# Kernel tuning notes

Hardware: AMD Instinct MI355X
Metric: run time of the kernel (lower is better)

The kernel has to match this reference:

```python
import jax, jax.numpy as jnp
from jax import lax
import numpy as np

EPSILON = 0.5
BETA = 1.0
N_ITER_FREE = 500
N_ITER_CLAMPED = 8


def setup_inputs() -> dict:
    key = jax.random.key(0)
    ks = jax.random.split(key, 12)
    B = 256
    x = jax.random.uniform(ks[0], (B, 784), dtype=jnp.float32)
    t = jax.random.uniform(ks[1], (B, 10), dtype=jnp.float32)
    u1 = jnp.zeros((B, 500), jnp.float32)
    u2 = jnp.zeros((B, 500), jnp.float32)
    u3 = jnp.zeros((B, 500), jnp.float32)
    u4 = jnp.zeros((B, 10), jnp.float32)
    a0 = np.float32(np.sqrt(2.0 / (784.0 + 500.0)))
    a1 = np.float32(np.sqrt(2.0 / (500.0 + 500.0)))
    a2 = np.float32(np.sqrt(2.0 / (500.0 + 10.0)))
    W0 = jax.random.normal(ks[2], (784, 500), jnp.float32) * a0
    b0 = jax.random.normal(ks[3], (500,), jnp.float32) * a0
    W1 = jax.random.normal(ks[4], (500, 500), jnp.float32) * a1
    b1 = jax.random.normal(ks[5], (500,), jnp.float32) * a1
    W2 = jax.random.normal(ks[6], (500, 500), jnp.float32) * a1
    b2 = jax.random.normal(ks[7], (500,), jnp.float32) * a1
    W3 = jax.random.normal(ks[8], (500, 10), jnp.float32) * a2
    b3 = jax.random.normal(ks[9], (10,), jnp.float32) * a2
    return dict(x=x, u1=u1, u2=u2, u3=u3, u4=u4, t=t,
                W0=W0, W1=W1, W2=W2, W3=W3, b0=b0, b1=b1, b2=b2, b3=b3)


def _rho(v):
    return jnp.clip(v, 0.0, 1.0)


def _d_rho(v):
    return ((v >= 0.0) & (v <= 1.0)).astype(v.dtype)


def reference(x, u1, u2, u3, u4, t, W0, W1, W2, W3, b0, b1, b2, b3):
    # x (units[0]) is clamped input; precompute its constant drive into layer 1.
    xW0 = x @ W0 + b0  # [B,500], invariant across iterations

    def deltas(c):
        u1, u2, u3, u4 = c
        # Jacobi update: all d_units use the pre-update states (matches torch code).
        d1 = _d_rho(u1) * (xW0 + u2 @ W1.T) - u1
        d2 = _d_rho(u2) * (u1 @ W1 + u3 @ W2.T + b1) - u2
        d3 = _d_rho(u3) * (u2 @ W2 + u4 @ W3.T + b2) - u3
        d4 = _d_rho(u4) * (u3 @ W3 + b3) - u4
        return d1, d2, d3, d4

    def free_step(c, _):
        d1, d2, d3, d4 = deltas(c)
        new = tuple(_rho(u + EPSILON * d) for u, d in zip(c, (d1, d2, d3, d4)))
        return new, None

    def clamped_step(c, _):
        d1, d2, d3, d4 = deltas(c)
        d4 = d4 + BETA * (t - c[3])
        new = tuple(_rho(u + EPSILON * d) for u, d in zip(c, (d1, d2, d3, d4)))
        return new, None

    units_free, _ = lax.scan(free_step, (u1, u2, u3, u4), None, length=N_ITER_FREE)
    units_clamped, _ = lax.scan(clamped_step, units_free, None, length=N_ITER_CLAMPED)
    # fixed_points returns (units_free, units_clamped); flatten the two phases.
    return (*units_free, *units_clamped)
```

## Files before the change

### kernel.cpp

```cpp
#include <hip/hip_runtime.h>


typedef float  f32x4 __attribute__((ext_vector_type(4)));
typedef short  s16x8 __attribute__((ext_vector_type(8)));
typedef short  s16x4 __attribute__((ext_vector_type(4)));
typedef unsigned int uint;
typedef uint   u32x4 __attribute__((ext_vector_type(4)));

#define MFMA_BF16 __builtin_amdgcn_mfma_f32_16x16x32_bf16

#define NFREE   500
#define NCLAMP  8
#define NITER   (NFREE + NCLAMP)
#define ROWLEN  1568
#define NSAMP   256
#define ROWTOT  (NSAMP * ROWLEN)

#define B1_OFF   0
#define B2A_OFF  262144
#define B2B_OFF  524288
#define B3A_OFF  786432
#define B3B_OFF  1048576
#define B4_OFF   1064960
#define BTOT     1081344

#define WS_UHL   0
#define WS_XW0   (WS_UHL + 2*ROWTOT*4)
#define WS_BIAS  (WS_XW0 + NSAMP*512*4)
#define WS_CNT   (WS_BIAS + 6400)
#define WS_BH    (WS_CNT + 1024)
#define WS_BL    (WS_BH + BTOT*2)
#define WS_END   (WS_BL + BTOT*2)

__device__ __forceinline__ short f2bf(float f){
  unsigned u = __float_as_uint(f);
  unsigned r = (u + 0x7FFFu + ((u >> 16) & 1u)) >> 16;
  return (short)r;
}
__device__ __forceinline__ float bf2f(short s){
  return __uint_as_float(((unsigned)(unsigned short)s) << 16);
}
__device__ __forceinline__ uint packbf(float v){
  short h = f2bf(v);
  short l = f2bf(v - bf2f(h));
  return (uint)(unsigned short)h | ((uint)(unsigned short)l << 16);
}

#define SYSLD(dst, addr) \
  asm volatile("global_load_dwordx4 %0, %1, off sc0 sc1" : "=v"(dst) : "v"(addr) : "memory")
__device__ __forceinline__ void store_sys(uint* p, uint v){
  asm volatile("global_store_dword %0, %1, off sc0 sc1" :: "v"(p), "v"(v) : "memory");
}
#define VMW_(N, X) do { \
  asm volatile("s_waitcnt vmcnt(" #N ")\n//%0" : "+v"(X) :: "memory"); \
  __builtin_amdgcn_sched_barrier(0); } while(0)
#define VMW(N, X) VMW_(N, X)
#define PRC(N, X, OFF) do { \
  VMW(N, X); \
  s16x4 h_ = (s16x4){ (short)((X)[0] & 0xffff), (short)((X)[1] & 0xffff), \
                      (short)((X)[2] & 0xffff), (short)((X)[3] & 0xffff) }; \
  s16x4 l_ = (s16x4){ (short)((X)[0] >> 16), (short)((X)[1] >> 16), \
                      (short)((X)[2] >> 16), (short)((X)[3] >> 16) }; \
  *(s16x4*)(L + (OFF)) = h_; *(s16x4*)(L + 32768 + (OFF)) = l_; } while(0)

#define BARRIER(ITV) do { \
  asm volatile("s_waitcnt vmcnt(0)" ::: "memory"); \
  __syncthreads(); \
  if (tid == 0){ \
    __hip_atomic_fetch_add(cg, 1u, __ATOMIC_RELAXED, __HIP_MEMORY_SCOPE_SYSTEM); \
    const unsigned tgt_ = 16u * (unsigned)((ITV) + 1); \
    while (__hip_atomic_load(cg, __ATOMIC_RELAXED, __HIP_MEMORY_SCOPE_SYSTEM) < tgt_){ \
      __builtin_amdgcn_s_sleep(1); \
    } \
  } \
  __syncthreads(); } while(0)

__global__ void initK(const float* __restrict__ u1, const float* __restrict__ u2,
                      const float* __restrict__ u3, const float* __restrict__ u4,
                      const float* __restrict__ b1, const float* __restrict__ b2,
                      uint* __restrict__ uhl, float* __restrict__ bias,
                      uint* __restrict__ cnt){
  const int b = blockIdx.x, tid = threadIdx.x;
  for (int col = tid; col < ROWLEN; col += 256){
    float v;
    if      (col < 512)  v = (col < 500)        ? u1[b*500 + col]        : 0.f;
    else if (col < 1024) v = ((col-512) < 500)  ? u2[b*500 + col - 512]  : 0.f;
    else if (col < 1536) v = ((col-1024) < 500) ? u3[b*500 + col - 1024] : 0.f;
    else                 v = ((col-1536) < 10)  ? u4[b*10 + col - 1536]  : 0.f;
    uhl[b*ROWLEN + col] = packbf(v);
    if (b == 0){
      float bv = 0.f;
      if      (col >= 512  && col < 1024){ int i = col-512;  if (i < 500) bv = b1[i]; }
      else if (col >= 1024 && col < 1536){ int i = col-1024; if (i < 500) bv = b2[i]; }
      bias[col] = bv;
    }
  }
  if (b == 0) cnt[tid] = 0;
}

__global__ void xw0K(const float* __restrict__ x, const float* __restrict__ W0,
                     const float* __restrict__ b0, float* __restrict__ xw0p){
  __shared__ float xs[784];
  const int b = blockIdx.x, tid = threadIdx.x;
  for (int j = tid; j < 784; j += 512) xs[j] = x[b*784 + j];
  __syncthreads();
  float a = 0.f;
  if (tid < 500){
    a = b0[tid];
    #pragma unroll 4
    for (int j = 0; j < 784; ++j) a = fmaf(xs[j], W0[j*500 + tid], a);
  }
  xw0p[b*512 + tid] = (tid < 500) ? a : 0.f;
}

__global__ void packK(const float* __restrict__ W1, const float* __restrict__ W2,
                      const float* __restrict__ W3, short* __restrict__ Bh,
                      short* __restrict__ Bl){
  const int bid = blockIdx.x, ln = threadIdx.x;
  int m, base, nks, poff;
  if      (bid < 512) { m=0; base=0;    nks=16; poff=B1_OFF;  }
  else if (bid < 1024){ m=1; base=512;  nks=16; poff=B2A_OFF; }
  else if (bid < 1536){ m=2; base=1024; nks=16; poff=B2B_OFF; }
  else if (bid < 2048){ m=3; base=1536; nks=16; poff=B3A_OFF; }
  else if (bid < 2080){ m=4; base=2048; nks=1;  poff=B3B_OFF; }
  else                { m=5; base=2080; nks=16; poff=B4_OFF;  }
  const int local = bid - base, ct = local / nks, ks = local % nks;
  short hv[8], lv[8];
  #pragma unroll
  for (int j = 0; j < 8; ++j){
    const int k = ks*32 + (ln>>4)*8 + j;
    const int c = ct*16 + (ln & 15);
    float v = 0.f;
    if      (m==0){ if (k<500 && c<500) v = W1[c*500 + k]; }
    else if (m==1){ if (k<500 && c<500) v = W1[k*500 + c]; }
    else if (m==2){ if (k<500 && c<500) v = W2[c*500 + k]; }
    else if (m==3){ if (k<500 && c<500) v = W2[k*500 + c]; }
    else if (m==4){ if (k<10  && c<500) v = W3[c*10  + k]; }
    else          { if (k<500 && c<10 ) v = W3[k*10  + c]; }
    short h = f2bf(v); hv[j] = h; lv[j] = f2bf(v - bf2f(h));
  }
  const int o = poff + (ct*nks + ks)*512 + ln*8;
  #pragma unroll
  for (int j = 0; j < 8; ++j){ Bh[o+j] = hv[j]; Bl[o+j] = lv[j]; }
}

__global__ void __launch_bounds__(256, 1) mainK(
    const short* __restrict__ Bh, const short* __restrict__ Bl,
    uint* __restrict__ uhl, const float* __restrict__ xw0p,
    const float* __restrict__ bias,
    const float* __restrict__ u1in, const float* __restrict__ u2in,
    const float* __restrict__ u3in, const float* __restrict__ u4in,
    const float* __restrict__ tin, const float* __restrict__ b3,
    float* __restrict__ dout, uint* __restrict__ cnt)
{
  __shared__ short ldss[32768];
  char* L = (char*)ldss;
  const int bid = blockIdx.x;
  const int rg  = bid & 15;
  const int tp  = bid >> 4;
  const int tid = threadIdx.x;
  const int wv  = tid >> 6, ln = tid & 63;
  const int lrow = ln & 15, lkg = ln >> 4;
  const int rowbase = rg * 16;
  const int sg16 = tid >> 4, l16 = tid & 15;
  const int abase = lrow*2048 + ((lkg*16) ^ ((lrow & 7) << 4));
  uint* cg = cnt + rg*16;

  if (tp < 8){
    s16x8 bh[32], bl[32];
    const int ctg = tp*4 + wv;
    #pragma unroll
    for (int ks = 0; ks < 32; ++ks){
      const int of = (ks < 16 ? B2A_OFF + (ctg*16 + ks)*512
                              : B2B_OFF + (ctg*16 + ks - 16)*512) + ln*8;
      bh[ks] = *(const s16x8*)(Bh + of);
      bl[ks] = *(const s16x8*)(Bl + of);
    }
    const int i0 = tp*64 + wv*16 + lrow;
    const int colg = 512 + i0;
    const float biasv = bias[colg];
    f32x4 uold, uold4;
    #pragma unroll
    for (int r = 0; r < 4; ++r){
      const int b = rowbase + lkg*4 + r;
      uold[r]  = (i0 < 500)   ? u2in[b*500 + i0]  : 0.f;
      uold4[r] = (lrow < 10)  ? u4in[b*10 + lrow] : 0.f;
    }
    const int rA = sg16 >> 1, half = sg16 & 1;
    const bool doU4 = (tp == 0 && wv == 0);

    for (int it = 0; it < NITER; ++it){
      const uint* uhlB = uhl + (size_t)(it & 1)*ROWTOT;
      uint*       uhlN = uhl + (size_t)((it & 1) ^ 1)*ROWTOT;
      const int snap = (it == NFREE-1) ? 0 : ((it == NITER-1) ? 386560 : -1);
      {
        const uint* sA = uhlB + (size_t)(rowbase + rA)*ROWLEN + half*1024 + l16*4;
        const uint* sB = sA + 8*ROWLEN;
        u32x4 a0,a1,a2,a3,a4,a5,a6,a7,c0,c1,c2,c3,c4,c5,c6,c7;
        SYSLD(a0, sA+0);   SYSLD(a1, sA+64);  SYSLD(a2, sA+128); SYSLD(a3, sA+192);
        SYSLD(a4, sA+256); SYSLD(a5, sA+320); SYSLD(a6, sA+384); SYSLD(a7, sA+448);
        SYSLD(c0, sB+0);   SYSLD(c1, sB+64);  SYSLD(c2, sB+128); SYSLD(c3, sB+192);
        SYSLD(c4, sB+256); SYSLD(c5, sB+320); SYSLD(c6, sB+384); SYSLD(c7, sB+448);
        const int obA = rA*2048 + ((half*1024 + l16*8) ^ ((rA & 7) << 4));
        const int obB = obA + 16384;
        PRC(15, a0, obA+0);   PRC(14, a1, obA+128); PRC(13, a2, obA+256); PRC(12, a3, obA+384);
        PRC(11, a4, obA+512); PRC(10, a5, obA+640); PRC(9,  a6, obA+768); PRC(8,  a7, obA+896);
        PRC(7,  c0, obB+0);   PRC(6,  c1, obB+128); PRC(5,  c2, obB+256); PRC(4,  c3, obB+384);
        PRC(3,  c4, obB+512); PRC(2,  c5, obB+640); PRC(1,  c6, obB+768); PRC(0,  c7, obB+896);
      }
      __syncthreads();
      f32x4 acc = {0.f,0.f,0.f,0.f};
      #pragma unroll
      for (int ks = 0; ks < 32; ++ks){
        const int off = abase ^ (ks*64);
        s16x8 aH = *(const s16x8*)(L + off);
        s16x8 aL = *(const s16x8*)(L + 32768 + off);
        acc = MFMA_BF16(aH, bh[ks], acc, 0, 0, 0);
        acc = MFMA_BF16(aH, bl[ks], acc, 0, 0, 0);
        acc = MFMA_BF16(aL, bh[ks], acc, 0, 0, 0);
      }
      f32x4 acc4 = {0.f,0.f,0.f,0.f};
      if (doU4){
        #pragma unroll
        for (int ks = 0; ks < 16; ++ks){
          const int off = (abase + 1024) ^ (ks*64);
          s16x8 aH = *(const s16x8*)(L + off);
          s16x8 aL = *(const s16x8*)(L + 32768 + off);
          const int of4 = B4_OFF + ks*512 + ln*8;
          s16x8 b4h = *(const s16x8*)(Bh + of4);
          s16x8 b4l = *(const s16x8*)(Bl + of4);
          acc4 = MFMA_BF16(aH, b4h, acc4, 0, 0, 0);
          acc4 = MFMA_BF16(aH, b4l, acc4, 0, 0, 0);
          acc4 = MFMA_BF16(aL, b4h, acc4, 0, 0, 0);
        }
      }
      #pragma unroll
      for (int r = 0; r < 4; ++r){
        const int b = rowbase + lkg*4 + r;
        const float y = acc[r] + biasv;
        float v = 0.5f*(uold[r] + y);
        v = fminf(fmaxf(v, 0.f), 1.f);
        if (i0 >= 500) v = 0.f;
        uold[r] = v;
        store_sys(uhlN + (size_t)b*ROWLEN + colg, packbf(v));
        if (snap >= 0 && i0 < 500) dout[snap + 128000 + b*500 + i0] = v;
      }
      if (doU4){
        const bool clamped = (it >= NFREE);
        #pragma unroll
        for (int r = 0; r < 4; ++r){
          const int b = rowbase + lkg*4 + r;
          float v = 0.f;
          if (lrow < 10){
            const float y = acc4[r] + b3[lrow];
            v = clamped ? 0.5f*(y + tin[b*10 + lrow]) : 0.5f*(uold4[r] + y);
            v = fminf(fmaxf(v, 0.f), 1.f);
          }
          uold4[r] = v;
          store_sys(uhlN + (size_t)b*ROWLEN + 1536 + lrow, packbf(v));
          store_sys(uhlN + (size_t)b*ROWLEN + 1552 + lrow, 0u);
          if (snap >= 0 && lrow < 10) dout[snap + 384000 + b*10 + lrow] = v;
        }
      }
      BARRIER(it);
    }
  } else {
    const bool IS3 = (tp >= 12);
    const int cbb  = IS3 ? (tp - 12) : (tp - 8);
    const int ct0  = cbb*8 + wv*2;
    s16x8 bh0[16], bl0[16], bh1[16], bl1[16];
    {
      const int base = IS3 ? B3A_OFF : B1_OFF;
      #pragma unroll
      for (int ks = 0; ks < 16; ++ks){
        const int ofA = base + ((ct0+0)*16 + ks)*512 + ln*8;
        const int ofB = base + ((ct0+1)*16 + ks)*512 + ln*8;
        bh0[ks] = *(const s16x8*)(Bh + ofA); bl0[ks] = *(const s16x8*)(Bl + ofA);
        bh1[ks] = *(const s16x8*)(Bh + ofB); bl1[ks] = *(const s16x8*)(Bl + ofB);
      }
    }
    s16x8 th0 = {0,0,0,0,0,0,0,0}, tl0 = th0, th1 = th0, tl1 = th0;
    if (IS3){
      th0 = *(const s16x8*)(Bh + B3B_OFF + (ct0+0)*512 + ln*8);
      tl0 = *(const s16x8*)(Bl + B3B_OFF + (ct0+0)*512 + ln*8);
      th1 = *(const s16x8*)(Bh + B3B_OFF + (ct0+1)*512 + ln*8);
      tl1 = *(const s16x8*)(Bl + B3B_OFF + (ct0+1)*512 + ln*8);
    }
    const int colg0 = (IS3 ? 1024 : 0) + cbb*128 + wv*32;
    const int iA = (colg0 & 511) + lrow, iB = iA + 16;
    const float biasA = bias[colg0 + lrow], biasB = bias[colg0 + 16 + lrow];
    const float* uin = IS3 ? u3in : u1in;
    f32x4 uoldA, uoldB;
    #pragma unroll
    for (int r = 0; r < 4; ++r){
      const int b = rowbase + lkg*4 + r;
      uoldA[r] = (iA < 500) ? uin[b*500 + iA] : 0.f;
      uoldB[r] = (iB < 500) ? uin[b*500 + iB] : 0.f;
    }
    const int dseg = IS3 ? 256000 : 0;

    for (int it = 0; it < NITER; ++it){
      const uint* uhlB = uhl + (size_t)(it & 1)*ROWTOT;
      uint*       uhlN = uhl + (size_t)((it & 1) ^ 1)*ROWTOT;
      const int snap = (it == NFREE-1) ? 0 : ((it == NITER-1) ? 386560 : -1);
      {
        const uint* sA = uhlB + (size_t)(rowbase + sg16)*ROWLEN + 512 + l16*4;
        u32x4 a0,a1,a2,a3,a4,a5,a6,a7;
        SYSLD(a0, sA+0);   SYSLD(a1, sA+64);  SYSLD(a2, sA+128); SYSLD(a3, sA+192);
        SYSLD(a4, sA+256); SYSLD(a5, sA+320); SYSLD(a6, sA+384); SYSLD(a7, sA+448);
        const int ob = sg16*2048 + ((l16*8) ^ ((sg16 & 7) << 4));
        if (tid < 128){
          const int row4 = tid >> 3, q = tid & 7;
          u32x4 c0;
          SYSLD(c0, uhlB + (size_t)(rowbase + row4)*ROWLEN + 1536 + q*4);
          PRC(8, a0, ob+0);   PRC(7, a1, ob+128); PRC(6, a2, ob+256); PRC(5, a3, ob+384);
          PRC(4, a4, ob+512); PRC(3, a5, ob+640); PRC(2, a6, ob+768); PRC(1, a7, ob+896);
          const int ob4 = row4*2048 + ((1024 + q*8) ^ ((row4 & 7) << 4));
          PRC(0, c0, ob4);
        } else {
          PRC(7, a0, ob+0);   PRC(6, a1, ob+128); PRC(5, a2, ob+256); PRC(4, a3, ob+384);
          PRC(3, a4, ob+512); PRC(2, a5, ob+640); PRC(1, a6, ob+768); PRC(0, a7, ob+896);
        }
      }
      __syncthreads();
      f32x4 accA = {0.f,0.f,0.f,0.f}, accB = {0.f,0.f,0.f,0.f};
      #pragma unroll
      for (int ks = 0; ks < 16; ++ks){
        const int off = abase ^ (ks*64);
        s16x8 aH = *(const s16x8*)(L + off);
        s16x8 aL = *(const s16x8*)(L + 32768 + off);
        accA = MFMA_BF16(aH, bh0[ks], accA, 0, 0, 0);
        accA = MFMA_BF16(aH, bl0[ks], accA, 0, 0, 0);
        accA = MFMA_BF16(aL, bh0[ks], accA, 0, 0, 0);
        accB = MFMA_BF16(aH, bh1[ks], accB, 0, 0, 0);
        accB = MFMA_BF16(aH, bl1[ks], accB, 0, 0, 0);
        accB = MFMA_BF16(aL, bh1[ks], accB, 0, 0, 0);
      }
      if (IS3){
        const int off = abase + 1024;
        s16x8 aH = *(const s16x8*)(L + off);
        s16x8 aL = *(const s16x8*)(L + 32768 + off);
        accA = MFMA_BF16(aH, th0, accA, 0, 0, 0);
        accA = MFMA_BF16(aH, tl0, accA, 0, 0, 0);
        accA = MFMA_BF16(aL, th0, accA, 0, 0, 0);
        accB = MFMA_BF16(aH, th1, accB, 0, 0, 0);
        accB = MFMA_BF16(aH, tl1, accB, 0, 0, 0);
        accB = MFMA_BF16(aL, th1, accB, 0, 0, 0);
      }
      #pragma unroll
      for (int r = 0; r < 4; ++r){
        const int b = rowbase + lkg*4 + r;
        {
          float y = accA[r] + biasA;
          if (!IS3) y += xw0p[b*512 + colg0 + lrow];
          float v = 0.5f*(uoldA[r] + y);
          v = fminf(fmaxf(v, 0.f), 1.f);
          if (iA >= 500) v = 0.f;
          uoldA[r] = v;
          store_sys(uhlN + (size_t)b*ROWLEN + colg0 + lrow, packbf(v));
          if (snap >= 0 && iA < 500) dout[snap + dseg + b*500 + iA] = v;
        }
        {
          float y = accB[r] + biasB;
          if (!IS3) y += xw0p[b*512 + colg0 + 16 + lrow];
          float v = 0.5f*(uoldB[r] + y);
          v = fminf(fmaxf(v, 0.f), 1.f);
          if (iB >= 500) v = 0.f;
          uoldB[r] = v;
          store_sys(uhlN + (size_t)b*ROWLEN + colg0 + 16 + lrow, packbf(v));
          if (snap >= 0 && iB < 500) dout[snap + dseg + b*500 + iB] = v;
        }
      }
      BARRIER(it);
    }
  }
}

extern "C" void kernel_launch(void* const* d_in, const int* in_sizes, int n_in,
                              void* d_out, int out_size, void* d_ws, size_t ws_size,
                              hipStream_t stream)
{
  const float* x  = (const float*)d_in[0];
  const float* u1 = (const float*)d_in[1];
  const float* u2 = (const float*)d_in[2];
  const float* u3 = (const float*)d_in[3];
  const float* u4 = (const float*)d_in[4];
  const float* t  = (const float*)d_in[5];
  const float* W0 = (const float*)d_in[6];
  const float* W1 = (const float*)d_in[7];
  const float* W2 = (const float*)d_in[8];
  const float* W3 = (const float*)d_in[9];
  const float* b0 = (const float*)d_in[10];
  const float* b1 = (const float*)d_in[11];
  const float* b2 = (const float*)d_in[12];
  const float* b3 = (const float*)d_in[13];

  char* ws = (char*)d_ws;
  uint*  uhl  = (uint*) (ws + WS_UHL);
  float* xw0p = (float*)(ws + WS_XW0);
  float* bias = (float*)(ws + WS_BIAS);
  uint*  cnt  = (uint*) (ws + WS_CNT);
  short* Bh   = (short*)(ws + WS_BH);
  short* Bl   = (short*)(ws + WS_BL);
  float* dout = (float*)d_out;

  initK<<<256, 256, 0, stream>>>(u1, u2, u3, u4, b1, b2, uhl, bias, cnt);
  xw0K<<<256, 512, 0, stream>>>(x, W0, b0, xw0p);
  packK<<<2112, 64, 0, stream>>>(W1, W2, W3, Bh, Bl);

  void* args[] = { &Bh, &Bl, &uhl, &xw0p, &bias,
                   &u1, &u2, &u3, &u4, &t, &b3, &dout, &cnt };
  hipError_t e = hipLaunchCooperativeKernel((const void*)mainK, dim3(256),
                                            dim3(256), args, 0, stream);
  if (e != hipSuccess){
    mainK<<<256, 256, 0, stream>>>(Bh, Bl, uhl, xw0p, bias,
                                   u1, u2, u3, u4, t, b3, dout, cnt);
  }
  (void)in_sizes; (void)n_in; (void)out_size; (void)ws_size;
}
```

Measured before the change: 3.987 ms.

## Split MFMA accumulators into independent chains and batch load waits

Each single accumulator chain of three dependent MFMAs is split into two accumulators, one for the high product and one for the correction terms, so consecutive MFMAs no longer serialize on one result. The per-load staggered vmcnt waits are replaced by a single wait for all loads before unpacking into LDS. The u4 MFMA block is moved ahead of the main loop. This shortens the MFMA dependency chains at the cost of extra accumulator registers, and gives up the overlap of unpacking with outstanding loads.

```diff
diff --git a/kernel.cpp b/kernel.cpp
--- a/kernel.cpp
+++ b/kernel.cpp
@@ -51,12 +51,10 @@
 __device__ __forceinline__ void store_sys(uint* p, uint v){
   asm volatile("global_store_dword %0, %1, off sc0 sc1" :: "v"(p), "v"(v) : "memory");
 }
-#define VMW_(N, X) do { \
-  asm volatile("s_waitcnt vmcnt(" #N ")\n//%0" : "+v"(X) :: "memory"); \
+#define WAITALL() do { \
+  asm volatile("s_waitcnt vmcnt(0)" ::: "memory"); \
   __builtin_amdgcn_sched_barrier(0); } while(0)
-#define VMW(N, X) VMW_(N, X)
-#define PRC(N, X, OFF) do { \
-  VMW(N, X); \
+#define UNPK(X, OFF) do { \
   s16x4 h_ = (s16x4){ (short)((X)[0] & 0xffff), (short)((X)[1] & 0xffff), \
                       (short)((X)[2] & 0xffff), (short)((X)[3] & 0xffff) }; \
   s16x4 l_ = (s16x4){ (short)((X)[0] >> 16), (short)((X)[1] >> 16), \
@@ -201,25 +199,16 @@
         SYSLD(a4, sA+256); SYSLD(a5, sA+320); SYSLD(a6, sA+384); SYSLD(a7, sA+448);
         SYSLD(c0, sB+0);   SYSLD(c1, sB+64);  SYSLD(c2, sB+128); SYSLD(c3, sB+192);
         SYSLD(c4, sB+256); SYSLD(c5, sB+320); SYSLD(c6, sB+384); SYSLD(c7, sB+448);
+        WAITALL();
         const int obA = rA*2048 + ((half*1024 + l16*8) ^ ((rA & 7) << 4));
         const int obB = obA + 16384;
-        PRC(15, a0, obA+0);   PRC(14, a1, obA+128); PRC(13, a2, obA+256); PRC(12, a3, obA+384);
-        PRC(11, a4, obA+512); PRC(10, a5, obA+640); PRC(9,  a6, obA+768); PRC(8,  a7, obA+896);
-        PRC(7,  c0, obB+0);   PRC(6,  c1, obB+128); PRC(5,  c2, obB+256); PRC(4,  c3, obB+384);
-        PRC(3,  c4, obB+512); PRC(2,  c5, obB+640); PRC(1,  c6, obB+768); PRC(0,  c7, obB+896);
+        UNPK(a0, obA+0);   UNPK(a1, obA+128); UNPK(a2, obA+256); UNPK(a3, obA+384);
+        UNPK(a4, obA+512); UNPK(a5, obA+640); UNPK(a6, obA+768); UNPK(a7, obA+896);
+        UNPK(c0, obB+0);   UNPK(c1, obB+128); UNPK(c2, obB+256); UNPK(c3, obB+384);
+        UNPK(c4, obB+512); UNPK(c5, obB+640); UNPK(c6, obB+768); UNPK(c7, obB+896);
       }
       __syncthreads();
-      f32x4 acc = {0.f,0.f,0.f,0.f};
-      #pragma unroll
-      for (int ks = 0; ks < 32; ++ks){
-        const int off = abase ^ (ks*64);
-        s16x8 aH = *(const s16x8*)(L + off);
-        s16x8 aL = *(const s16x8*)(L + 32768 + off);
-        acc = MFMA_BF16(aH, bh[ks], acc, 0, 0, 0);
-        acc = MFMA_BF16(aH, bl[ks], acc, 0, 0, 0);
-        acc = MFMA_BF16(aL, bh[ks], acc, 0, 0, 0);
-      }
-      f32x4 acc4 = {0.f,0.f,0.f,0.f};
+      f32x4 h4 = {0.f,0.f,0.f,0.f}, x4 = {0.f,0.f,0.f,0.f};
       if (doU4){
         #pragma unroll
         for (int ks = 0; ks < 16; ++ks){
@@ -229,15 +218,25 @@
           const int of4 = B4_OFF + ks*512 + ln*8;
           s16x8 b4h = *(const s16x8*)(Bh + of4);
           s16x8 b4l = *(const s16x8*)(Bl + of4);
-          acc4 = MFMA_BF16(aH, b4h, acc4, 0, 0, 0);
-          acc4 = MFMA_BF16(aH, b4l, acc4, 0, 0, 0);
-          acc4 = MFMA_BF16(aL, b4h, acc4, 0, 0, 0);
+          h4 = MFMA_BF16(aH, b4h, h4, 0, 0, 0);
+          x4 = MFMA_BF16(aH, b4l, x4, 0, 0, 0);
+          x4 = MFMA_BF16(aL, b4h, x4, 0, 0, 0);
         }
+      }
+      f32x4 acch = {0.f,0.f,0.f,0.f}, accx = {0.f,0.f,0.f,0.f};
+      #pragma unroll
+      for (int ks = 0; ks < 32; ++ks){
+        const int off = abase ^ (ks*64);
+        s16x8 aH = *(const s16x8*)(L + off);
+        s16x8 aL = *(const s16x8*)(L + 32768 + off);
+        acch = MFMA_BF16(aH, bh[ks], acch, 0, 0, 0);
+        accx = MFMA_BF16(aH, bl[ks], accx, 0, 0, 0);
+        accx = MFMA_BF16(aL, bh[ks], accx, 0, 0, 0);
       }
       #pragma unroll
       for (int r = 0; r < 4; ++r){
         const int b = rowbase + lkg*4 + r;
-        const float y = acc[r] + biasv;
+        const float y = acch[r] + accx[r] + biasv;
         float v = 0.5f*(uold[r] + y);
         v = fminf(fmaxf(v, 0.f), 1.f);
         if (i0 >= 500) v = 0.f;
@@ -252,7 +251,7 @@
           const int b = rowbase + lkg*4 + r;
           float v = 0.f;
           if (lrow < 10){
-            const float y = acc4[r] + b3[lrow];
+            const float y = h4[r] + x4[r] + b3[lrow];
             v = clamped ? 0.5f*(y + tin[b*10 + lrow]) : 0.5f*(uold4[r] + y);
             v = fminf(fmaxf(v, 0.f), 1.f);
           }
@@ -305,53 +304,52 @@
       const int snap = (it == NFREE-1) ? 0 : ((it == NITER-1) ? 386560 : -1);
       {
         const uint* sA = uhlB + (size_t)(rowbase + sg16)*ROWLEN + 512 + l16*4;
-        u32x4 a0,a1,a2,a3,a4,a5,a6,a7;
+        u32x4 a0,a1,a2,a3,a4,a5,a6,a7, c0;
         SYSLD(a0, sA+0);   SYSLD(a1, sA+64);  SYSLD(a2, sA+128); SYSLD(a3, sA+192);
         SYSLD(a4, sA+256); SYSLD(a5, sA+320); SYSLD(a6, sA+384); SYSLD(a7, sA+448);
+        const int row4 = tid >> 3, q = tid & 7;
+        if (tid < 128)
+          SYSLD(c0, uhlB + (size_t)(rowbase + row4)*ROWLEN + 1536 + q*4);
+        WAITALL();
         const int ob = sg16*2048 + ((l16*8) ^ ((sg16 & 7) << 4));
+        UNPK(a0, ob+0);   UNPK(a1, ob+128); UNPK(a2, ob+256); UNPK(a3, ob+384);
+        UNPK(a4, ob+512); UNPK(a5, ob+640); UNPK(a6, ob+768); UNPK(a7, ob+896);
         if (tid < 128){
-          const int row4 = tid >> 3, q = tid & 7;
-          u32x4 c0;
-          SYSLD(c0, uhlB + (size_t)(rowbase + row4)*ROWLEN + 1536 + q*4);
-          PRC(8, a0, ob+0);   PRC(7, a1, ob+128); PRC(6, a2, ob+256); PRC(5, a3, ob+384);
-          PRC(4, a4, ob+512); PRC(3, a5, ob+640); PRC(2, a6, ob+768); PRC(1, a7, ob+896);
           const int ob4 = row4*2048 + ((1024 + q*8) ^ ((row4 & 7) << 4));
-          PRC(0, c0, ob4);
-        } else {
-          PRC(7, a0, ob+0);   PRC(6, a1, ob+128); PRC(5, a2, ob+256); PRC(4, a3, ob+384);
-          PRC(3, a4, ob+512); PRC(2, a5, ob+640); PRC(1, a6, ob+768); PRC(0, a7, ob+896);
+          UNPK(c0, ob4);
         }
       }
       __syncthreads();
-      f32x4 accA = {0.f,0.f,0.f,0.f}, accB = {0.f,0.f,0.f,0.f};
+      f32x4 hA = {0.f,0.f,0.f,0.f}, xA = {0.f,0.f,0.f,0.f};
+      f32x4 hB = {0.f,0.f,0.f,0.f}, xB = {0.f,0.f,0.f,0.f};
       #pragma unroll
       for (int ks = 0; ks < 16; ++ks){
         const int off = abase ^ (ks*64);
         s16x8 aH = *(const s16x8*)(L + off);
         s16x8 aL = *(const s16x8*)(L + 32768 + off);
-        accA = MFMA_BF16(aH, bh0[ks], accA, 0, 0, 0);
-        accA = MFMA_BF16(aH, bl0[ks], accA, 0, 0, 0);
-        accA = MFMA_BF16(aL, bh0[ks], accA, 0, 0, 0);
-        accB = MFMA_BF16(aH, bh1[ks], accB, 0, 0, 0);
-        accB = MFMA_BF16(aH, bl1[ks], accB, 0, 0, 0);
-        accB = MFMA_BF16(aL, bh1[ks], accB, 0, 0, 0);
+        hA = MFMA_BF16(aH, bh0[ks], hA, 0, 0, 0);
+        xA = MFMA_BF16(aH, bl0[ks], xA, 0, 0, 0);
+        xA = MFMA_BF16(aL, bh0[ks], xA, 0, 0, 0);
+        hB = MFMA_BF16(aH, bh1[ks], hB, 0, 0, 0);
+        xB = MFMA_BF16(aH, bl1[ks], xB, 0, 0, 0);
+        xB = MFMA_BF16(aL, bh1[ks], xB, 0, 0, 0);
       }
       if (IS3){
         const int off = abase + 1024;
         s16x8 aH = *(const s16x8*)(L + off);
         s16x8 aL = *(const s16x8*)(L + 32768 + off);
-        accA = MFMA_BF16(aH, th0, accA, 0, 0, 0);
-        accA = MFMA_BF16(aH, tl0, accA, 0, 0, 0);
-        accA = MFMA_BF16(aL, th0, accA, 0, 0, 0);
-        accB = MFMA_BF16(aH, th1, accB, 0, 0, 0);
-        accB = MFMA_BF16(aH, tl1, accB, 0, 0, 0);
-        accB = MFMA_BF16(aL, th1, accB, 0, 0, 0);
+        hA = MFMA_BF16(aH, th0, hA, 0, 0, 0);
+        xA = MFMA_BF16(aH, tl0, xA, 0, 0, 0);
+        xA = MFMA_BF16(aL, th0, xA, 0, 0, 0);
+        hB = MFMA_BF16(aH, th1, hB, 0, 0, 0);
+        xB = MFMA_BF16(aH, tl1, xB, 0, 0, 0);
+        xB = MFMA_BF16(aL, th1, xB, 0, 0, 0);
       }
       #pragma unroll
       for (int r = 0; r < 4; ++r){
         const int b = rowbase + lkg*4 + r;
         {
-          float y = accA[r] + biasA;
+          float y = hA[r] + xA[r] + biasA;
           if (!IS3) y += xw0p[b*512 + colg0 + lrow];
           float v = 0.5f*(uoldA[r] + y);
           v = fminf(fmaxf(v, 0.f), 1.f);
@@ -361,7 +359,7 @@
           if (snap >= 0 && iA < 500) dout[snap + dseg + b*500 + iA] = v;
         }
         {
-          float y = accB[r] + biasB;
+          float y = hB[r] + xB[r] + biasB;
           if (!IS3) y += xw0p[b*512 + colg0 + 16 + lrow];
           float v = 0.5f*(uoldB[r] + y);
           v = fminf(fmaxf(v, 0.f), 1.f);
```

Result: no change. 3.996 ms (+0.2%).
